# Kernel tuning notes

Measured on AMD Instinct MI355X. Metric: run time of the kernel, lower is better.

## Reference

```python
import jax, jax.numpy as jnp
import numpy as np

B, N, MAX_DEG = 256, 512, 6
F_IN, H = 62, 128  # layers = [62, 128, 128]
NUM_DEG = MAX_DEG + 1  # degree buckets 0..6


def gather_neighbors(atoms, edges, maskvalue):
    # atoms [B,N,F], edges [B,N,D] with -1 padding -> [B,N,D,F]
    idx = jnp.maximum(edges, 0)
    neigh = jax.vmap(lambda a, e: a[e])(atoms, idx)
    return jnp.where(edges[..., None] < 0, jnp.asarray(maskvalue, atoms.dtype), neigh)


def nfp_conv(atoms, edges, W, b):
    # W [NUM_DEG, F_in, F_out], b [NUM_DEG, F_out]
    deg = jnp.sum(edges >= 0, axis=-1)  # [B,N]
    neigh = gather_neighbors(atoms, edges, 0.0)
    summed = neigh.sum(axis=2) + atoms  # include self, [B,N,F_in]
    out = jnp.zeros(summed.shape[:2] + (W.shape[-1],), summed.dtype)
    for d in range(NUM_DEG):  # small fixed set of degree buckets
        h = jax.nn.sigmoid(summed @ W[d] + b[d])
        out = out + h * (deg == d)[..., None].astype(h.dtype)
    return out


def graph_pool(atoms, edges):
    # max over self + neighbors
    neigh = gather_neighbors(atoms, edges, -jnp.inf)
    allf = jnp.concatenate([atoms[:, :, None, :], neigh], axis=2)  # [B,N,D+1,F]
    return allf.max(axis=2)


def setup_inputs() -> dict:
    key = jax.random.key(0)
    ka, ke, km, k0, k1, k2, k3 = jax.random.split(key, 7)
    a = jax.random.normal(ka, (B, N, F_IN), dtype=jnp.float32)
    e = jax.random.randint(ke, (B, N, MAX_DEG), 0, N, dtype=jnp.int32)
    # introduce -1 padding so atoms have varied degrees 0..6
    u = jax.random.uniform(km, (B, N, MAX_DEG))
    e = jnp.where(u < 0.6, e, -1).astype(jnp.int32)
    W0 = jax.random.normal(k0, (NUM_DEG, F_IN, H), dtype=jnp.float32) * 0.1
    b0 = jax.random.normal(k1, (NUM_DEG, H), dtype=jnp.float32) * 0.1
    W1 = jax.random.normal(k2, (NUM_DEG, H, H), dtype=jnp.float32) * 0.1
    b1 = jax.random.normal(k3, (NUM_DEG, H), dtype=jnp.float32) * 0.1
    return {"a": a, "e": e, "W0": W0, "b0": b0, "W1": W1, "b1": b1}


def reference(a, e, W0, b0, W1, b1):
    x = nfp_conv(a, e, W0, b0)
    x = graph_pool(x, e)
    x = nfp_conv(x, e, W1, b1)
    x = graph_pool(x, e)
    return x.sum(axis=1)  # SubgraphSum: [B, H]
```

## Files before the change

### kernel.cpp

```cpp
#include <hip/hip_runtime.h>
#include <math.h>

#define BB 256
#define NN 512
#define DD 6
#define F_IN 62
#define HH 128
#define ND 7
#define TOTAL (BB*NN)
#define OPB 640
#define GPB 40
#define TPB 10

typedef __bf16 bf16x8 __attribute__((ext_vector_type(8)));
typedef float f32x4 __attribute__((ext_vector_type(4)));

__device__ __forceinline__ unsigned short f2bf(float f) {
    unsigned u = __builtin_bit_cast(unsigned, f);
    u = (u + 0x7FFFu + ((u >> 16) & 1u)) >> 16;
    return (unsigned short)u;
}
__device__ __forceinline__ float lo2f(unsigned x) { return __builtin_bit_cast(float, x << 16); }
__device__ __forceinline__ float hi2f(unsigned x) { return __builtin_bit_cast(float, x & 0xFFFF0000u); }

__device__ __forceinline__ uint4 pack8(const float* s) {
    uint4 r;
    r.x = (unsigned)f2bf(s[0]) | ((unsigned)f2bf(s[1]) << 16);
    r.y = (unsigned)f2bf(s[2]) | ((unsigned)f2bf(s[3]) << 16);
    r.z = (unsigned)f2bf(s[4]) | ((unsigned)f2bf(s[5]) << 16);
    r.w = (unsigned)f2bf(s[6]) | ((unsigned)f2bf(s[7]) << 16);
    return r;
}
__device__ __forceinline__ void unpack_add(float* s, uint4 q) {
    s[0] += lo2f(q.x); s[1] += hi2f(q.x); s[2] += lo2f(q.y); s[3] += hi2f(q.y);
    s[4] += lo2f(q.z); s[5] += hi2f(q.z); s[6] += lo2f(q.w); s[7] += hi2f(q.w);
}
__device__ __forceinline__ void unpack_max(float* s, uint4 q) {
    s[0] = fmaxf(s[0], lo2f(q.x)); s[1] = fmaxf(s[1], hi2f(q.x));
    s[2] = fmaxf(s[2], lo2f(q.y)); s[3] = fmaxf(s[3], hi2f(q.y));
    s[4] = fmaxf(s[4], lo2f(q.z)); s[5] = fmaxf(s[5], hi2f(q.z));
    s[6] = fmaxf(s[6], lo2f(q.w)); s[7] = fmaxf(s[7], hi2f(q.w));
}


__global__ __launch_bounds__(512) void k_sort16(const int* __restrict__ e,
                                                int* __restrict__ order,
                                                int* __restrict__ dgrp,
                                                int* __restrict__ ntiles) {
    __shared__ unsigned int scnt[ND];
    __shared__ unsigned int sbase[ND + 1];
    const int b = blockIdx.x;
    const int t = threadIdx.x;
    if (t < ND) scnt[t] = 0u;
    for (int i = t; i < OPB; i += 512) order[b * OPB + i] = -1;
    __syncthreads();
    int d = 0;
#pragma unroll
    for (int j = 0; j < DD; ++j) d += (e[(b * NN + t) * DD + j] >= 0) ? 1 : 0;
    unsigned rk = atomicAdd(&scnt[d], 1u);
    __syncthreads();
    if (t == 0) {
        unsigned acc = 0;
        for (int k = 0; k < ND; ++k) { sbase[k] = acc; acc += (scnt[k] + 15u) & ~15u; }
        sbase[ND] = acc;
        for (int k = 0; k < ND; ++k)
            for (unsigned g = sbase[k] >> 4; g < (sbase[k + 1] >> 4); ++g)
                dgrp[b * GPB + g] = k;
        for (unsigned g = acc >> 4; g < GPB; ++g) dgrp[b * GPB + g] = 0;
        ntiles[b] = (int)((acc + 63u) >> 6);
    }
    __syncthreads();
    order[b * OPB + sbase[d] + rk] = t;
}


__global__ void k_prep_wt(const float* __restrict__ W, unsigned short* __restrict__ WT,
                          int F, int K) {
    int n = blockIdx.x;
    int d = blockIdx.y;
    for (int k = threadIdx.x; k < K; k += 64) {
        float v = (k < F) ? W[((size_t)d * F + k) * HH + n] : 0.f;
        WT[((size_t)d * HH + n) * K + k] = f2bf(v);
    }
}


__global__ __launch_bounds__(512)
void k_gather1(const float* __restrict__ a, const int* __restrict__ e,
               const int* __restrict__ order, const int* __restrict__ ntiles,
               unsigned short* __restrict__ S1) {
    const int t = threadIdx.x;
    const int bi = blockIdx.x;
    const int x8 = bi & 7;
    const int j = bi >> 3;
    const int batch = x8 + 8 * (j / TPB);
    const int blk = j % TPB;
    if (blk >= ntiles[batch]) return;
    const int slot = blk * 64 + (t >> 3);
    const int kb = t & 7;
    const int v = order[batch * OPB + slot];
    if (v < 0) return;
    const int* ep = e + ((size_t)batch * NN + v) * DD;
    const float* base = a + (size_t)batch * NN * F_IN;
    float s[8] = {0.f, 0.f, 0.f, 0.f, 0.f, 0.f, 0.f, 0.f};
    {
        const float* r = base + (size_t)v * F_IN + kb * 8;
        float2 z0 = *(const float2*)(r);     s[0] += z0.x; s[1] += z0.y;
        float2 z1 = *(const float2*)(r + 2); s[2] += z1.x; s[3] += z1.y;
        float2 z2 = *(const float2*)(r + 4); s[4] += z2.x; s[5] += z2.y;
        if (kb < 7) { float2 z3 = *(const float2*)(r + 6); s[6] += z3.x; s[7] += z3.y; }
    }
#pragma unroll
    for (int jj = 0; jj < DD; ++jj) {
        int idx = ep[jj];
        if (idx >= 0) {
            const float* r = base + (size_t)idx * F_IN + kb * 8;
            float2 z0 = *(const float2*)(r);     s[0] += z0.x; s[1] += z0.y;
            float2 z1 = *(const float2*)(r + 2); s[2] += z1.x; s[3] += z1.y;
            float2 z2 = *(const float2*)(r + 4); s[4] += z2.x; s[5] += z2.y;
            if (kb < 7) { float2 z3 = *(const float2*)(r + 6); s[6] += z3.x; s[7] += z3.y; }
        }
    }
    *(uint4*)(S1 + ((size_t)batch * OPB + slot) * 64 + kb * 8) = pack8(s);
}


__global__ __launch_bounds__(512)
void k_gather2(const unsigned short* __restrict__ P1, const int* __restrict__ e,
               const int* __restrict__ order, const int* __restrict__ ntiles,
               unsigned short* __restrict__ S2m, unsigned short* __restrict__ S2p) {
    constexpr int BPB2 = 20;
    const int t = threadIdx.x;
    const int bi = blockIdx.x;
    const int x8 = bi & 7;
    const int j = bi >> 3;
    const int batch = x8 + 8 * (j / BPB2);
    const int blk = j % BPB2;
    if ((blk >> 1) >= ntiles[batch]) return;
    const int slot = blk * 32 + (t >> 4);
    const int kb = t & 15;
    const int v = order[batch * OPB + slot];
    if (v < 0) return;
    const int* ep = e + ((size_t)batch * NN + v) * DD;
    const unsigned short* base = P1 + (size_t)batch * NN * HH + kb * 8;
    float s[8] = {0.f, 0.f, 0.f, 0.f, 0.f, 0.f, 0.f, 0.f};
    unpack_add(s, *(const uint4*)(base + (size_t)v * HH));
#pragma unroll
    for (int jj = 0; jj < DD; ++jj) {
        int idx = ep[jj];
        if (idx >= 0) unpack_add(s, *(const uint4*)(base + (size_t)idx * HH));
    }
    uint4 r = pack8(s);
    if (slot < 512) *(uint4*)(S2m + ((size_t)batch * 512 + slot) * HH + kb * 8) = r;
    else            *(uint4*)(S2p + ((size_t)batch * 128 + (slot - 512)) * HH + kb * 8) = r;
}


template<int KB>
__global__ __launch_bounds__(512, 4)
void k_gemm(const unsigned short* __restrict__ Sm, const unsigned short* __restrict__ Sp,
            const unsigned short* __restrict__ WT, const float* __restrict__ bias,
            const int* __restrict__ order, const int* __restrict__ dgrp,
            const int* __restrict__ ntiles, unsigned short* __restrict__ Y) {
    constexpr int K = KB * 8;
    constexpr int LOGKB = (KB == 16) ? 4 : 3;
    __shared__ unsigned short sP[64 * 128];
    __shared__ int vT[64];

    const int t = threadIdx.x;
    const int l = t & 63;
    const int w = t >> 6;

    const int bi = blockIdx.x;
    const int x8 = bi & 7;
    const int j = bi >> 3;
    const int batch = x8 + 8 * (j / TPB);
    const int tile = j % TPB;
    if (tile >= ntiles[batch]) return;

    if (t < 64) vT[t] = order[batch * OPB + tile * 64 + t];

    for (int u = t; u < 64 * KB; u += 512) {
        const int n = u >> LOGKB;
        const int kb = u & (KB - 1);
        const int slot = tile * 64 + n;
        const unsigned short* src;
        if constexpr (KB == 16) {
            src = (slot < 512) ? Sm + ((size_t)batch * 512 + slot) * K + kb * 8
                               : Sp + ((size_t)batch * 128 + (slot - 512)) * K + kb * 8;
        } else {
            src = Sm + ((size_t)batch * OPB + slot) * K + kb * 8;
        }
        *(uint4*)&sP[(n * KB + (kb ^ (n & 7))) * 8] = *(const uint4*)src;
    }
    __syncthreads();

    const int lr = l & 15;
    const int lq = l >> 4;
    const int mb = w >> 1;
    const int col0 = (w & 1) * 64;
    const int d = dgrp[batch * GPB + tile * 4 + mb];
    const int nrow = mb * 16 + lr;

    bf16x8 af[K / 32];
#pragma unroll
    for (int kk = 0; kk < K / 32; ++kk)
        af[kk] = *(const bf16x8*)&sP[(nrow * KB + ((kk * 4 + lq) ^ (nrow & 7))) * 8];

    f32x4 acc[4];
#pragma unroll
    for (int fr = 0; fr < 4; ++fr) { f32x4 z = {0.f, 0.f, 0.f, 0.f}; acc[fr] = z; }
#pragma unroll
    for (int fr = 0; fr < 4; ++fr) {
        const unsigned short* wp = WT + ((size_t)d * HH + col0 + fr * 16 + lr) * K + lq * 8;
#pragma unroll
        for (int kk = 0; kk < K / 32; ++kk) {
            bf16x8 bfr = *(const bf16x8*)(wp + kk * 32);
            acc[fr] = __builtin_amdgcn_mfma_f32_16x16x32_bf16(af[kk], bfr, acc[fr], 0, 0, 0);
        }
    }

    __syncthreads();
#pragma unroll
    for (int fr = 0; fr < 4; ++fr) {
        const int col = col0 + fr * 16 + lr;
        const float bv = bias[d * HH + col];
#pragma unroll
        for (int r = 0; r < 4; ++r) {
            const int n = mb * 16 + lq * 4 + r;
            float z = 1.f / (1.f + __expf(-(acc[fr][r] + bv)));
            sP[n * HH + col] = f2bf(z);
        }
    }
    __syncthreads();
    for (int u = t; u < 1024; u += 512) {
        int n = u >> 4;
        int c8 = (u & 15) * 8;
        int v = vT[n];
        if (v >= 0) {
            uint4 p = *(const uint4*)&sP[n * HH + c8];
            *(uint4*)&Y[((size_t)batch * NN + v) * HH + c8] = p;
        }
    }
}


__global__ __launch_bounds__(256) void k_pool_bf(const unsigned short* __restrict__ X,
                                                 const int* __restrict__ e,
                                                 unsigned short* __restrict__ P) {
    const int t = threadIdx.x;
    const int bi = blockIdx.x;
    const int x8 = bi & 7;
    const int j = bi >> 3;
    const int batch = x8 + 8 * (j >> 5);
    const int sub = j & 31;
    const int u = batch * NN + sub * 16 + (t >> 4);
    const int c8 = (t & 15) * 8;
    const int nbase = u & ~(NN - 1);
    float m[8];
    {
        uint4 p = *(const uint4*)(X + (size_t)u * HH + c8);
        m[0] = lo2f(p.x); m[1] = hi2f(p.x); m[2] = lo2f(p.y); m[3] = hi2f(p.y);
        m[4] = lo2f(p.z); m[5] = hi2f(p.z); m[6] = lo2f(p.w); m[7] = hi2f(p.w);
    }
#pragma unroll
    for (int jj = 0; jj < DD; ++jj) {
        int idx = e[u * DD + jj];
        if (idx >= 0) unpack_max(m, *(const uint4*)(X + (size_t)(nbase + idx) * HH + c8));
    }
    *(uint4*)&P[(size_t)u * HH + c8] = pack8(m);
}


__global__ __launch_bounds__(256) void k_pool_sum_part(const unsigned short* __restrict__ X,
                                                       const int* __restrict__ e,
                                                       float* __restrict__ partial) {
    __shared__ float red[16][HH + 4];
    const int t = threadIdx.x;
    const int bi = blockIdx.x;
    const int x8 = bi & 7;
    const int j = bi >> 3;
    const int b = x8 + 8 * (j >> 5);
    const int chunk = j & 31;
    const int slot = t >> 4;
    const int c8 = (t & 15) * 8;

    const int u = b * NN + chunk * 16 + slot;
    float m[8];
    {
        uint4 p = *(const uint4*)(X + (size_t)u * HH + c8);
        m[0] = lo2f(p.x); m[1] = hi2f(p.x); m[2] = lo2f(p.y); m[3] = hi2f(p.y);
        m[4] = lo2f(p.z); m[5] = hi2f(p.z); m[6] = lo2f(p.w); m[7] = hi2f(p.w);
    }
#pragma unroll
    for (int jj = 0; jj < DD; ++jj) {
        int idx = e[u * DD + jj];
        if (idx >= 0) unpack_max(m, *(const uint4*)(X + (size_t)(b * NN + idx) * HH + c8));
    }
#pragma unroll
    for (int i = 0; i < 8; ++i) red[slot][c8 + i] = m[i];
    __syncthreads();
    if (t < HH) {
        float s = 0.f;
#pragma unroll
        for (int k = 0; k < 16; ++k) s += red[k][t];
        partial[((size_t)b * 32 + chunk) * HH + t] = s;
    }
}


__global__ __launch_bounds__(256) void k_sum_final(const float* __restrict__ partial,
                                                   float* __restrict__ out) {
    int g = blockIdx.x * 256 + threadIdx.x;
    int b = g >> 7;
    int c = g & 127;
    float s = 0.f;
#pragma unroll
    for (int k = 0; k < 32; ++k) s += partial[((size_t)b * 32 + k) * HH + c];
    out[g] = s;
}


extern "C" void kernel_launch(void* const* d_in, const int* in_sizes, int n_in,
                              void* d_out, int out_size, void* d_ws, size_t ws_size,
                              hipStream_t stream) {
    const float* a  = (const float*)d_in[0];
    const int*   e  = (const int*)d_in[1];
    const float* W0 = (const float*)d_in[2];
    const float* b0 = (const float*)d_in[3];
    const float* W1 = (const float*)d_in[4];
    const float* b1 = (const float*)d_in[5];
    float* out = (float*)d_out;

    char* ws = (char*)d_ws;
    const size_t MB32 = (size_t)TOTAL * HH * 2;
    unsigned short* bufA = (unsigned short*)ws;
    unsigned short* bufB = (unsigned short*)(ws + MB32);
    unsigned short* S2p  = (unsigned short*)(ws + 2 * MB32);
    float* partial = (float*)S2p;
    char* dp = ws + 2 * MB32 + (size_t)BB * 128 * HH * 2;
    unsigned short* WT0 = (unsigned short*)dp;
    unsigned short* WT1 = WT0 + (size_t)ND * HH * 64;
    int* order  = (int*)(WT1 + (size_t)ND * HH * 128);
    int* dgrp   = order + (size_t)BB * OPB;
    int* ntiles = dgrp + (size_t)BB * GPB;

    hipLaunchKernelGGL(k_sort16, dim3(BB), dim3(NN), 0, stream, e, order, dgrp, ntiles);
    hipLaunchKernelGGL(k_prep_wt, dim3(HH, ND), dim3(64), 0, stream, W0, WT0, F_IN, 64);
    hipLaunchKernelGGL(k_prep_wt, dim3(HH, ND), dim3(64), 0, stream, W1, WT1, HH, HH);

    hipLaunchKernelGGL(k_gather1, dim3(BB * TPB), dim3(512), 0, stream,
                       a, e, order, ntiles, bufB);
    hipLaunchKernelGGL((k_gemm<8>), dim3(BB * TPB), dim3(512), 0, stream,
                       bufB, (const unsigned short*)nullptr, WT0, b0, order, dgrp, ntiles, bufA);
    hipLaunchKernelGGL(k_pool_bf, dim3(TOTAL / 16), dim3(256), 0, stream, bufA, e, bufB);
    hipLaunchKernelGGL(k_gather2, dim3(BB * 20), dim3(512), 0, stream,
                       bufB, e, order, ntiles, bufA, S2p);
    hipLaunchKernelGGL((k_gemm<16>), dim3(BB * TPB), dim3(512), 0, stream,
                       bufA, S2p, WT1, b1, order, dgrp, ntiles, bufB);
    hipLaunchKernelGGL(k_pool_sum_part, dim3(BB * 32), dim3(256), 0, stream, bufB, e, partial);
    hipLaunchKernelGGL(k_sum_final, dim3(BB * HH / 256), dim3(256), 0, stream, partial, out);
}
```

Before: 172.5 us.

## Keep GEMM outputs in degree-sorted slot order and pool via inverse permutation

The GEMM kernels now write results contiguously in degree-sorted slot order (OPBS=624 slots per batch) rather than scattering rows back to node order through the order table. The pooling kernels instead look up each node's slot through a new inverse-permutation array built in the sort kernel. Gather2 writes one unified sorted buffer instead of splitting it into main and overflow parts. This makes GEMM stores coalesced and removes the vT indirection, at the cost of an extra inv[] lookup per neighbor in the pooling gathers.

```diff
diff --git a/kernel.cpp b/kernel.cpp
--- a/kernel.cpp
+++ b/kernel.cpp
@@ -9,6 +9,7 @@
 #define ND 7
 #define TOTAL (BB*NN)
 #define OPB 640
+#define OPBS 624
 #define GPB 40
 #define TPB 10
 
@@ -45,6 +46,7 @@
 
 __global__ __launch_bounds__(512) void k_sort16(const int* __restrict__ e,
                                                 int* __restrict__ order,
+                                                int* __restrict__ inv,
                                                 int* __restrict__ dgrp,
                                                 int* __restrict__ ntiles) {
     __shared__ unsigned int scnt[ND];
@@ -66,11 +68,13 @@
         for (int k = 0; k < ND; ++k)
             for (unsigned g = sbase[k] >> 4; g < (sbase[k + 1] >> 4); ++g)
                 dgrp[b * GPB + g] = k;
-        for (unsigned g = acc >> 4; g < GPB; ++g) dgrp[b * GPB + g] = 0;
-        ntiles[b] = (int)((acc + 63u) >> 6);
-    }
-    __syncthreads();
-    order[b * OPB + sbase[d] + rk] = t;
+        for (unsigned g = sbase[ND] >> 4; g < GPB; ++g) dgrp[b * GPB + g] = 0;
+        ntiles[b] = (int)((sbase[ND] + 63u) >> 6);
+    }
+    __syncthreads();
+    const int slot = (int)(sbase[d] + rk);
+    order[b * OPB + slot] = t;
+    inv[b * NN + t] = slot;
 }
 
 
@@ -121,14 +125,14 @@
             if (kb < 7) { float2 z3 = *(const float2*)(r + 6); s[6] += z3.x; s[7] += z3.y; }
         }
     }
-    *(uint4*)(S1 + ((size_t)batch * OPB + slot) * 64 + kb * 8) = pack8(s);
+    *(uint4*)(S1 + ((size_t)batch * OPBS + slot) * 64 + kb * 8) = pack8(s);
 }
 
 
 __global__ __launch_bounds__(512)
 void k_gather2(const unsigned short* __restrict__ P1, const int* __restrict__ e,
                const int* __restrict__ order, const int* __restrict__ ntiles,
-               unsigned short* __restrict__ S2m, unsigned short* __restrict__ S2p) {
+               unsigned short* __restrict__ S2) {
     constexpr int BPB2 = 20;
     const int t = threadIdx.x;
     const int bi = blockIdx.x;
@@ -150,22 +154,19 @@
         int idx = ep[jj];
         if (idx >= 0) unpack_add(s, *(const uint4*)(base + (size_t)idx * HH));
     }
-    uint4 r = pack8(s);
-    if (slot < 512) *(uint4*)(S2m + ((size_t)batch * 512 + slot) * HH + kb * 8) = r;
-    else            *(uint4*)(S2p + ((size_t)batch * 128 + (slot - 512)) * HH + kb * 8) = r;
+    *(uint4*)(S2 + ((size_t)batch * OPBS + slot) * HH + kb * 8) = pack8(s);
 }
 
 
 template<int KB>
 __global__ __launch_bounds__(512, 4)
-void k_gemm(const unsigned short* __restrict__ Sm, const unsigned short* __restrict__ Sp,
+void k_gemm(const unsigned short* __restrict__ S,
             const unsigned short* __restrict__ WT, const float* __restrict__ bias,
-            const int* __restrict__ order, const int* __restrict__ dgrp,
-            const int* __restrict__ ntiles, unsigned short* __restrict__ Y) {
+            const int* __restrict__ dgrp, const int* __restrict__ ntiles,
+            unsigned short* __restrict__ Y) {
     constexpr int K = KB * 8;
     constexpr int LOGKB = (KB == 16) ? 4 : 3;
     __shared__ unsigned short sP[64 * 128];
-    __shared__ int vT[64];
 
     const int t = threadIdx.x;
     const int l = t & 63;
@@ -178,19 +179,12 @@
     const int tile = j % TPB;
     if (tile >= ntiles[batch]) return;
 
-    if (t < 64) vT[t] = order[batch * OPB + tile * 64 + t];
-
     for (int u = t; u < 64 * KB; u += 512) {
         const int n = u >> LOGKB;
         const int kb = u & (KB - 1);
-        const int slot = tile * 64 + n;
-        const unsigned short* src;
-        if constexpr (KB == 16) {
-            src = (slot < 512) ? Sm + ((size_t)batch * 512 + slot) * K + kb * 8
-                               : Sp + ((size_t)batch * 128 + (slot - 512)) * K + kb * 8;
-        } else {
-            src = Sm + ((size_t)batch * OPB + slot) * K + kb * 8;
-        }
+        int slot = tile * 64 + n;
+        if (slot >= OPBS) slot = OPBS - 1;
+        const unsigned short* src = S + ((size_t)batch * OPBS + slot) * K + kb * 8;
         *(uint4*)&sP[(n * KB + (kb ^ (n & 7))) * 8] = *(const uint4*)src;
     }
     __syncthreads();
@@ -234,19 +228,20 @@
     }
     __syncthreads();
     for (int u = t; u < 1024; u += 512) {
-        int n = u >> 4;
-        int c8 = (u & 15) * 8;
-        int v = vT[n];
-        if (v >= 0) {
+        const int n = u >> 4;
+        const int c8 = (u & 15) * 8;
+        const int slot = tile * 64 + n;
+        if (slot < OPBS) {
             uint4 p = *(const uint4*)&sP[n * HH + c8];
-            *(uint4*)&Y[((size_t)batch * NN + v) * HH + c8] = p;
+            *(uint4*)&Y[((size_t)batch * OPBS + slot) * HH + c8] = p;
         }
     }
 }
 
 
-__global__ __launch_bounds__(256) void k_pool_bf(const unsigned short* __restrict__ X,
+__global__ __launch_bounds__(256) void k_pool_bf(const unsigned short* __restrict__ Xs,
                                                  const int* __restrict__ e,
+                                                 const int* __restrict__ inv,
                                                  unsigned short* __restrict__ P) {
     const int t = threadIdx.x;
     const int bi = blockIdx.x;
@@ -254,26 +249,28 @@
     const int j = bi >> 3;
     const int batch = x8 + 8 * (j >> 5);
     const int sub = j & 31;
-    const int u = batch * NN + sub * 16 + (t >> 4);
+    const int node = sub * 16 + (t >> 4);
+    const int u = batch * NN + node;
     const int c8 = (t & 15) * 8;
-    const int nbase = u & ~(NN - 1);
+    const unsigned short* base = Xs + (size_t)batch * OPBS * HH + c8;
     float m[8];
     {
-        uint4 p = *(const uint4*)(X + (size_t)u * HH + c8);
+        uint4 p = *(const uint4*)(base + (size_t)inv[u] * HH);
         m[0] = lo2f(p.x); m[1] = hi2f(p.x); m[2] = lo2f(p.y); m[3] = hi2f(p.y);
         m[4] = lo2f(p.z); m[5] = hi2f(p.z); m[6] = lo2f(p.w); m[7] = hi2f(p.w);
     }
 #pragma unroll
     for (int jj = 0; jj < DD; ++jj) {
         int idx = e[u * DD + jj];
-        if (idx >= 0) unpack_max(m, *(const uint4*)(X + (size_t)(nbase + idx) * HH + c8));
+        if (idx >= 0) unpack_max(m, *(const uint4*)(base + (size_t)inv[batch * NN + idx] * HH));
     }
     *(uint4*)&P[(size_t)u * HH + c8] = pack8(m);
 }
 
 
-__global__ __launch_bounds__(256) void k_pool_sum_part(const unsigned short* __restrict__ X,
+__global__ __launch_bounds__(256) void k_pool_sum_part(const unsigned short* __restrict__ Xs,
                                                        const int* __restrict__ e,
+                                                       const int* __restrict__ inv,
                                                        float* __restrict__ partial) {
     __shared__ float red[16][HH + 4];
     const int t = threadIdx.x;
@@ -286,16 +283,17 @@
     const int c8 = (t & 15) * 8;
 
     const int u = b * NN + chunk * 16 + slot;
+    const unsigned short* base = Xs + (size_t)b * OPBS * HH + c8;
     float m[8];
     {
-        uint4 p = *(const uint4*)(X + (size_t)u * HH + c8);
+        uint4 p = *(const uint4*)(base + (size_t)inv[u] * HH);
         m[0] = lo2f(p.x); m[1] = hi2f(p.x); m[2] = lo2f(p.y); m[3] = hi2f(p.y);
         m[4] = lo2f(p.z); m[5] = hi2f(p.z); m[6] = lo2f(p.w); m[7] = hi2f(p.w);
     }
 #pragma unroll
     for (int jj = 0; jj < DD; ++jj) {
         int idx = e[u * DD + jj];
-        if (idx >= 0) unpack_max(m, *(const uint4*)(X + (size_t)(b * NN + idx) * HH + c8));
+        if (idx >= 0) unpack_max(m, *(const uint4*)(base + (size_t)inv[b * NN + idx] * HH));
     }
 #pragma unroll
     for (int i = 0; i < 8; ++i) red[slot][c8 + i] = m[i];
@@ -333,31 +331,31 @@
     float* out = (float*)d_out;
 
     char* ws = (char*)d_ws;
-    const size_t MB32 = (size_t)TOTAL * HH * 2;
+    const size_t SB = (size_t)BB * OPBS * HH * 2;
     unsigned short* bufA = (unsigned short*)ws;
-    unsigned short* bufB = (unsigned short*)(ws + MB32);
-    unsigned short* S2p  = (unsigned short*)(ws + 2 * MB32);
-    float* partial = (float*)S2p;
-    char* dp = ws + 2 * MB32 + (size_t)BB * 128 * HH * 2;
+    unsigned short* bufB = (unsigned short*)(ws + SB);
+    float* partial = (float*)bufA;
+    char* dp = ws + 2 * SB;
     unsigned short* WT0 = (unsigned short*)dp;
     unsigned short* WT1 = WT0 + (size_t)ND * HH * 64;
     int* order  = (int*)(WT1 + (size_t)ND * HH * 128);
     int* dgrp   = order + (size_t)BB * OPB;
     int* ntiles = dgrp + (size_t)BB * GPB;
-
-    hipLaunchKernelGGL(k_sort16, dim3(BB), dim3(NN), 0, stream, e, order, dgrp, ntiles);
+    int* inv    = ntiles + 256;
+
+    hipLaunchKernelGGL(k_sort16, dim3(BB), dim3(NN), 0, stream, e, order, inv, dgrp, ntiles);
     hipLaunchKernelGGL(k_prep_wt, dim3(HH, ND), dim3(64), 0, stream, W0, WT0, F_IN, 64);
     hipLaunchKernelGGL(k_prep_wt, dim3(HH, ND), dim3(64), 0, stream, W1, WT1, HH, HH);
 
     hipLaunchKernelGGL(k_gather1, dim3(BB * TPB), dim3(512), 0, stream,
                        a, e, order, ntiles, bufB);
     hipLaunchKernelGGL((k_gemm<8>), dim3(BB * TPB), dim3(512), 0, stream,
-                       bufB, (const unsigned short*)nullptr, WT0, b0, order, dgrp, ntiles, bufA);
-    hipLaunchKernelGGL(k_pool_bf, dim3(TOTAL / 16), dim3(256), 0, stream, bufA, e, bufB);
+                       bufB, WT0, b0, dgrp, ntiles, bufA);
+    hipLaunchKernelGGL(k_pool_bf, dim3(TOTAL / 16), dim3(256), 0, stream, bufA, e, inv, bufB);
     hipLaunchKernelGGL(k_gather2, dim3(BB * 20), dim3(512), 0, stream,
-                       bufB, e, order, ntiles, bufA, S2p);
+                       bufB, e, order, ntiles, bufA);
     hipLaunchKernelGGL((k_gemm<16>), dim3(BB * TPB), dim3(512), 0, stream,
-                       bufA, S2p, WT1, b1, order, dgrp, ntiles, bufB);
-    hipLaunchKernelGGL(k_pool_sum_part, dim3(BB * 32), dim3(256), 0, stream, bufB, e, partial);
+                       bufA, WT1, b1, dgrp, ntiles, bufB);
+    hipLaunchKernelGGL(k_pool_sum_part, dim3(BB * 32), dim3(256), 0, stream, bufB, e, inv, partial);
     hipLaunchKernelGGL(k_sum_final, dim3(BB * HH / 256), dim3(256), 0, stream, partial, out);
 }
```

New measurement: 181.0 us. 5.0% more time.
